# Kernel optimization log

Measured on AMD Instinct MI355X. Metric: run time of the kernel, lower is better.

The kernel has to match this reference:

```python
import jax, jax.numpy as jnp
import numpy as np
from jax import lax

BN_EPS = 1e-5
TINY = 1e-12


def conv2d(x, w, stride, padding):
    # NCHW x OIHW -> NCHW
    return lax.conv_general_dilated(
        x, w, (stride, stride), [(padding, padding), (padding, padding)],
        dimension_numbers=('NCHW', 'OIHW', 'NCHW'))


def pool2x2(x):
    B, C, H, W = x.shape
    return x.reshape(B, C, H // 2, 2, W // 2, 2).mean(axis=(3, 5))


def setup_inputs() -> dict:
    key = jax.random.key(0)
    k0, k1, k2, k3 = jax.random.split(key, 4)
    B, Cin, H, W = 32, 128, 56, 56
    Cout, K = 256, 3
    mean = jax.random.normal(k0, (B, Cin, H, W), jnp.float32)
    std = jax.random.uniform(k1, (B, Cin, H, W), jnp.float32)  # std must be >= 0
    fan_in = Cin * K * K
    bound = 1.0 / np.sqrt(fan_in)  # torch Conv2d default init
    conv_w = jax.random.uniform(k2, (Cout, Cin, K, K), jnp.float32, -bound, bound)
    conv_b = jax.random.uniform(k3, (Cout,), jnp.float32, -bound, bound)
    bn_gamma = jnp.full((Cout,), 2.5, jnp.float32)  # module fills weight with 2.5
    bn_beta = jnp.full((Cout,), 2.5, jnp.float32)   # module fills bias with 2.5
    return {'mean': mean, 'std': std, 'conv_w': conv_w, 'conv_b': conv_b,
            'bn_gamma': bn_gamma, 'bn_beta': bn_beta}


def reference(mean, std, conv_w, conv_b, bn_gamma, bn_beta):
    # mean branch: standard conv
    m = conv2d(mean, conv_w, 1, 1) + conv_b[None, :, None, None]
    # std branch (no rho): independent-variance propagation, var -> conv with w^2
    var = conv2d(std * std, conv_w * conv_w, 1, 1)
    s = jnp.sqrt(var + TINY)
    # BatchNorm2d in training mode: batch statistics over (N, H, W)
    mu = jnp.mean(m, axis=(0, 2, 3), keepdims=True)
    v = jnp.var(m, axis=(0, 2, 3), keepdims=True)  # biased, like torch normalization
    inv = 1.0 / jnp.sqrt(v + BN_EPS)
    g = bn_gamma[None, :, None, None]
    uhat = (m - mu) * inv * g + bn_beta[None, :, None, None]
    # std through BN: pure linear scale by |gamma| / sqrt(var + eps)
    shat = s * inv * jnp.abs(g)
    # moment activation (erf-based Gaussian->Heaviside moment mapping)
    z = uhat / (shat * np.sqrt(2.0) + TINY)
    u = 0.5 * (1.0 + lax.erf(z))               # output mean in (0, 1)
    sa = jnp.sqrt(jnp.clip(u * (1.0 - u), TINY))  # output std of Bernoulli-like moments
    # avg-pool 2x2 stride 2: mean pools linearly, independent vars: std = sqrt(avg(var))/2
    u_p = pool2x2(u)
    s_p = jnp.sqrt(pool2x2(sa * sa)) * 0.5
    return (u_p, s_p)
```

## Files before the change

### kernel.cpp

```cpp
#include <hip/hip_runtime.h>
#include <hip/hip_bf16.h>
#include <math.h>

#define BB 32
#define CIN 128
#define HH 56
#define WW 56
#define COUT 256
#define HW (HH*WW)
#define NPIX (BB*HW)
#define PH 28
#define PW 28
#define POOL_ELEMS ((long)BB*COUT*PH*PW)
#define PADH 58
#define PADW 58
#define TRANS_BLOCKS ((BB*PADH*PADW*16)/256)
#define WPACK_BLOCKS ((9*COUT*CIN)/256)

typedef unsigned short u16;
using s16x8 = __attribute__((ext_vector_type(8))) short;
using s16x4 = __attribute__((ext_vector_type(4))) short;
using f32x4 = __attribute__((ext_vector_type(4))) float;

__device__ __forceinline__ float b2f(u16 u){ return __uint_as_float(((unsigned)u)<<16); }
__device__ __forceinline__ u16 f2b(float x){
    unsigned u = __float_as_uint(x);
    unsigned r = (u + 0x7fffu + ((u>>16)&1u)) >> 16;
    return (u16)r;
}

__device__ __forceinline__ void gload16(const void* g, void* l){
    __builtin_amdgcn_global_load_lds(
        (const __attribute__((address_space(1))) unsigned int*)g,
        (__attribute__((address_space(3))) unsigned int*)l, 16, 0, 0);
}


__global__ __launch_bounds__(256) void prep_kernel(
    const float* __restrict__ mean, const float* __restrict__ stdv,
    const float* __restrict__ w,
    u16* __restrict__ mean_pad, u16* __restrict__ std2_pad,
    u16* __restrict__ BP, u16* __restrict__ BP2)
{
    int bid = blockIdx.x;
    if (bid < TRANS_BLOCKS){
        int t   = bid*256 + threadIdx.x;
        int oct = t & 15;
        int pp  = t >> 4;
        int pw = pp % PADW; int tmp = pp / PADW;
        int ph = tmp % PADH; int b = tmp / PADH;
        size_t obase = (size_t)pp*CIN + oct*8;
        s16x8 pm = (s16x8){0,0,0,0,0,0,0,0}, ps = pm;
        if (ph >= 1 && ph <= HH && pw >= 1 && pw <= WW){
            long ibase = ((long)(b*CIN + oct*8)*HH + (ph-1))*WW + (pw-1);
            #pragma unroll
            for (int j=0;j<8;j++){
                float m = mean[ibase + (long)j*HW];
                float s = stdv[ibase + (long)j*HW];
                pm[j] = (short)f2b(m);
                ps[j] = (short)f2b(s*s);
            }
        }
        *(s16x8*)(mean_pad + obase) = pm;
        *(s16x8*)(std2_pad + obase) = ps;
    } else {
        int t = (bid - TRANS_BLOCKS)*256 + threadIdx.x;
        int e    = t & 7;
        int co   = (t >> 3) & 255;
        int rest = t >> 11;
        int ks   = rest >> 2;
        int sub  = rest & 3;
        int r    = ks >> 2;
        int ci   = (ks & 3)*32 + sub*8 + e;
        float v = w[((long)co*CIN + ci)*9 + r];
        BP[t]  = f2b(v);
        BP2[t] = f2b(v*v);
    }
}

__global__ __launch_bounds__(256,2) void convw_kernel(
    const u16* __restrict__ mean_pad, const u16* __restrict__ std2_pad,
    const u16* __restrict__ BP, const u16* __restrict__ BP2,
    const float* __restrict__ bias,
    u16* __restrict__ m_out, u16* __restrict__ v_out,
    float* __restrict__ sum_, float* __restrict__ sumsq_)
{
    __shared__ u16 lds[32768];
    const int tid  = threadIdx.x;
    const int lane = tid & 63;
    const int wv   = tid >> 6;

    int gid   = blockIdx.x;
    int local = gid >> 3;
    int p     = (gid & 7)*112 + (local >> 1);
    int path  = local & 1;
    const int b  = p / 28;
    const int h0 = (p - b*28) * 2;

    const u16* __restrict__ Ap = path ? std2_pad : mean_pad;
    const u16* __restrict__ Bp = path ? BP2      : BP;
    u16*       __restrict__ Op = path ? v_out    : m_out;

    const int slot_g = (tid & 15) ^ ((tid >> 4) & 15);
    const int wbase  = (b*PADH + h0)*PADW*CIN;
    const int athr   = (tid >> 4)*CIN + slot_g*8;
    #pragma unroll
    for (int i=0; i<16; ++i){
        const int Ci = (i>>2)*(PADW*CIN) + (i&3)*16*CIN;
        gload16(Ap + wbase + Ci + athr, &lds[i*2048 + tid*8]);
    }
    __syncthreads();

    int R0[7];
    #pragma unroll
    for (int mi=0; mi<7; ++mi){
        int px = mi*16 + (lane & 15);
        int dh = (px >= 56) ? 1 : 0;
        R0[mi] = dh*64 + (px - dh*56);
    }
    const int q = lane >> 4;

    const u16* bp = Bp + (size_t)((lane>>4)*256 + wv*64 + (lane&15))*8;

    f32x4 acc[7][4];
    #pragma unroll
    for (int i=0;i<7;i++)
      #pragma unroll
      for (int j=0;j<4;j++) acc[i][j] = (f32x4){0,0,0,0};

    #pragma unroll
    for (int r=0; r<9; ++r){
        const int kh = r/3, kw = r - (r/3)*3;

        int ab[7];
        #pragma unroll
        for (int mi=0; mi<7; ++mi){
            int R   = R0[mi] + kh*64 + kw;
            int t15 = (R0[mi] + kw) & 15;
            ab[mi] = R*128 + ((q ^ t15) << 3);
        }

        #pragma unroll
        for (int hf=0; hf<2; ++hf){
            #pragma unroll
            for (int kk=0; kk<2; ++kk){
                const size_t ksoff = (size_t)(r*4 + hf*2 + kk)*8192;
                s16x8 bf0 = *(const s16x8*)(bp + ksoff);
                s16x8 bf1 = *(const s16x8*)(bp + ksoff + 128);
                s16x8 bf2 = *(const s16x8*)(bp + ksoff + 256);
                s16x8 bf3 = *(const s16x8*)(bp + ksoff + 384);
                const int sx = hf*64 + kk*32;
                s16x8 af[7];
                #pragma unroll
                for (int mi=0; mi<7; ++mi)
                    af[mi] = *(const s16x8*)&lds[ab[mi] ^ sx];
                __builtin_amdgcn_s_setprio(1);
                #pragma unroll
                for (int mi=0; mi<7; ++mi){
                    acc[mi][0] = __builtin_amdgcn_mfma_f32_16x16x32_bf16(af[mi], bf0, acc[mi][0], 0,0,0);
                    acc[mi][1] = __builtin_amdgcn_mfma_f32_16x16x32_bf16(af[mi], bf1, acc[mi][1], 0,0,0);
                    acc[mi][2] = __builtin_amdgcn_mfma_f32_16x16x32_bf16(af[mi], bf2, acc[mi][2], 0,0,0);
                    acc[mi][3] = __builtin_amdgcn_mfma_f32_16x16x32_bf16(af[mi], bf3, acc[mi][3], 0,0,0);
                }
                __builtin_amdgcn_s_setprio(0);
            }
        }
    }

    float bv[4];
    if (path == 0){
        #pragma unroll
        for (int ni=0;ni<4;ni++) bv[ni] = bias[wv*64 + ni*16 + (lane&15)];
    } else {
        #pragma unroll
        for (int ni=0;ni<4;ni++) bv[ni] = 0.f;
    }

    float ssum[4] = {0.f,0.f,0.f,0.f}, ssq[4] = {0.f,0.f,0.f,0.f};

    #pragma unroll
    for (int mi=0; mi<7; ++mi){
        int px = mi*16 + ((lane>>4)<<2);
        int dh = (px >= 56) ? 1 : 0;
        int w  = px - dh*56;
        #pragma unroll
        for (int ni=0; ni<4; ++ni){
            int co = wv*64 + ni*16 + (lane&15);
            size_t o = (size_t)(b*COUT + co)*HW + (size_t)(h0+dh)*WW + w;
            s16x4 pk;
            #pragma unroll
            for (int rr=0; rr<4; ++rr){
                float vv = acc[mi][ni][rr] + bv[ni];
                pk[rr] = (short)f2b(vv);
                ssum[ni] += vv;
                ssq[ni]  += vv*vv;
            }
            *(s16x4*)(Op + o) = pk;
        }
    }

    if (path == 0){
        #pragma unroll
        for (int ni=0; ni<4; ++ni){
            float s = ssum[ni], s2 = ssq[ni];
            s  += __shfl_xor(s, 16, 64);  s2 += __shfl_xor(s2, 16, 64);
            s  += __shfl_xor(s, 32, 64);  s2 += __shfl_xor(s2, 32, 64);
            if (lane < 16){
                int co = wv*64 + ni*16 + lane;
                atomicAdd(&sum_[co],   s);
                atomicAdd(&sumsq_[co], s2);
            }
        }
    }
}

__global__ __launch_bounds__(256) void final_kernel(
        const u16* __restrict__ m, const u16* __restrict__ var,
        const float* __restrict__ sum_, const float* __restrict__ sumsq_,
        const float* __restrict__ gamma, const float* __restrict__ beta,
        float* __restrict__ out){
    int idx4 = blockIdx.x*256 + threadIdx.x;
    int wo4 = idx4 % (PW/4); int t = idx4 / (PW/4);
    int ho = t % PH; t /= PH;
    int co = t % COUT; int b = t / COUT;
    float g  = gamma[co];
    float be = beta[co];
    float mu = sum_[co] / (float)NPIX;
    float vr = sumsq_[co] / (float)NPIX - mu*mu;
    float inv = 1.0f / sqrtf(vr + 1e-5f);
    float ag = fabsf(g);
    float us[4] = {0.f,0.f,0.f,0.f}, ss[4] = {0.f,0.f,0.f,0.f};
    #pragma unroll
    for (int dh=0; dh<2; ++dh){
        long base = ((long)(b*COUT+co)*HH + 2*ho+dh)*WW + wo4*8;
        const s16x8 vm = *(const s16x8*)&m[base];
        const s16x8 vv = *(const s16x8*)&var[base];
        #pragma unroll
        for (int j=0;j<8;j++){
            float mm = b2f((u16)vm[j]);
            float sdev = sqrtf(b2f((u16)vv[j]) + 1e-12f);
            float uhat = (mm - mu)*inv*g + be;
            float shat = sdev*inv*ag;
            float z = uhat / (shat*1.41421356237f + 1e-12f);
            float u = 0.5f*(1.f + erff(z));
            us[j>>1] += u;
            ss[j>>1] += fmaxf(u*(1.f-u), 1e-12f);
        }
    }
    long ob = ((long)(b*COUT+co)*PH + ho)*PW + wo4*4;
    f32x4 o0, o1;
    #pragma unroll
    for (int k=0;k<4;k++){
        o0[k] = 0.25f*us[k];
        o1[k] = sqrtf(0.25f*ss[k])*0.5f;
    }
    *(f32x4*)(out + ob) = o0;
    *(f32x4*)(out + POOL_ELEMS + ob) = o1;
}


__global__ void wtransf_kernel(const float* __restrict__ w, float* __restrict__ wT){
    int out = blockIdx.x*256 + threadIdx.x;
    if (out >= COUT*CIN*9) return;
    int co = out % COUT;
    int r  = out / COUT;
    wT[out] = w[(long)co*(CIN*9) + r];
}

__global__ __launch_bounds__(256) void stats_old_kernel(const u16* __restrict__ m,
        float* __restrict__ mu_out, float* __restrict__ inv_out){
    int co = blockIdx.x;
    float s=0.f, s2=0.f;
    for (int oc = threadIdx.x; oc < NPIX/8; oc += 256){
        int b = oc / (HW/8); int o8 = oc - b*(HW/8);
        const s16x8 v8 = *(const s16x8*)&m[((size_t)(b*COUT+co))*HW + (size_t)o8*8];
        #pragma unroll
        for (int j=0;j<8;j++){ float v = b2f((u16)v8[j]); s += v; s2 += v*v; }
    }
    __shared__ float rs[256], rs2[256];
    rs[threadIdx.x]=s; rs2[threadIdx.x]=s2; __syncthreads();
    for (int o=128;o>0;o>>=1){
        if (threadIdx.x < o){ rs[threadIdx.x]+=rs[threadIdx.x+o]; rs2[threadIdx.x]+=rs2[threadIdx.x+o]; }
        __syncthreads();
    }
    if (threadIdx.x==0){
        float mu = rs[0]/(float)NPIX;
        float var = rs2[0]/(float)NPIX - mu*mu;
        mu_out[co] = mu;
        inv_out[co] = 1.0f/sqrtf(var + 1e-5f);
    }
}

__global__ __launch_bounds__(256) void final_old_kernel(
        const u16* __restrict__ m, const u16* __restrict__ var,
        const float* __restrict__ mu_, const float* __restrict__ inv_,
        const float* __restrict__ gamma, const float* __restrict__ beta,
        float* __restrict__ out){
    long idx = (long)blockIdx.x*256 + threadIdx.x;
    int wo = (int)(idx % PW); long t = idx / PW;
    int ho = (int)(t % PH); t /= PH;
    int co = (int)(t % COUT); int b = (int)(t / COUT);
    float g  = gamma[co];
    float be = beta[co];
    float mu = mu_[co], inv = inv_[co];
    float ag = fabsf(g);
    float us = 0.f, ss = 0.f;
    #pragma unroll
    for (int dh=0; dh<2; ++dh){
        int hpos = 2*ho+dh;
        long base = ((long)(b*COUT+co)*HH + hpos)*WW + 2*wo;
        #pragma unroll
        for (int dw=0; dw<2; ++dw){
            float mm = b2f(m[base+dw]);
            float vv = b2f(var[base+dw]);
            float sdev = sqrtf(vv + 1e-12f);
            float uhat = (mm - mu)*inv*g + be;
            float shat = sdev*inv*ag;
            float z = uhat / (shat*1.41421356237f + 1e-12f);
            float u = 0.5f*(1.f + erff(z));
            float sa2 = fmaxf(u*(1.f-u), 1e-12f);
            us += u; ss += sa2;
        }
    }
    out[idx]              = 0.25f*us;
    out[POOL_ELEMS + idx] = sqrtf(0.25f*ss)*0.5f;
}

#define CI_CHUNK 64
#define XW 32
__global__ __launch_bounds__(256) void conv_old_kernel(
    const float* __restrict__ mean, const float* __restrict__ stdv,
    const float* __restrict__ wT, const float* __restrict__ bias,
    u16* __restrict__ m_out, u16* __restrict__ v_out)
{
    __shared__ float lds_m[CI_CHUNK][3][XW];
    __shared__ float lds_s[CI_CHUNK][3][XW];
    const int co   = threadIdx.x;
    const int half = blockIdx.x;
    const int h    = blockIdx.y;
    const int b    = blockIdx.z;
    const int w_base = half*28;

    float acc_m[28], acc_v[28];
    #pragma unroll
    for (int i=0;i<28;i++){ acc_m[i]=0.f; acc_v[i]=0.f; }

    for (int c=0; c<CIN; c+=CI_CHUNK){
        for (int t = threadIdx.x; t < CI_CHUNK*3*30; t += 256){
            int pos = t % 30; int r = t / 30; int hh = r % 3; int ci_l = r / 3;
            int gh = h - 1 + hh; int gw = w_base - 1 + pos;
            float vm = 0.f, vs = 0.f;
            if ((unsigned)gh < (unsigned)HH && (unsigned)gw < (unsigned)WW){
                long gi = ((long)(b*CIN + (c+ci_l))*HH + gh)*WW + gw;
                vm = mean[gi];
                float sv = stdv[gi];
                vs = sv*sv;
            }
            lds_m[ci_l][hh][pos] = vm;
            lds_s[ci_l][hh][pos] = vs;
        }
        __syncthreads();
        for (int ci_l=0; ci_l<CI_CHUNK; ++ci_l){
            int rbase = (c+ci_l)*9;
            #pragma unroll
            for (int kh=0; kh<3; ++kh){
                float w0 = wT[(long)(rbase + kh*3 + 0)*COUT + co];
                float w1 = wT[(long)(rbase + kh*3 + 1)*COUT + co];
                float w2 = wT[(long)(rbase + kh*3 + 2)*COUT + co];
                float xm[30];
                #pragma unroll
                for (int p=0;p<30;p++) xm[p] = lds_m[ci_l][kh][p];
                #pragma unroll
                for (int i=0;i<28;i++) acc_m[i] += w0*xm[i] + w1*xm[i+1] + w2*xm[i+2];
                float q0=w0*w0, q1=w1*w1, q2=w2*w2;
                float xs[30];
                #pragma unroll
                for (int p=0;p<30;p++) xs[p] = lds_s[ci_l][kh][p];
                #pragma unroll
                for (int i=0;i<28;i++) acc_v[i] += q0*xs[i] + q1*xs[i+1] + q2*xs[i+2];
            }
        }
        __syncthreads();
    }
    float bvv = bias[co];
    long obase = ((long)(b*COUT+co)*HH + h)*WW + w_base;
    #pragma unroll
    for (int i=0;i<28;i++){
        m_out[obase+i] = f2b(acc_m[i]+bvv);
        v_out[obase+i] = f2b(acc_v[i]);
    }
}

extern "C" void kernel_launch(void* const* d_in, const int* in_sizes, int n_in,
                              void* d_out, int out_size, void* d_ws, size_t ws_size,
                              hipStream_t stream)
{
    const float* mean   = (const float*)d_in[0];
    const float* stdv   = (const float*)d_in[1];
    const float* conv_w = (const float*)d_in[2];
    const float* conv_b = (const float*)d_in[3];
    const float* gamma  = (const float*)d_in[4];
    const float* beta   = (const float*)d_in[5];
    float* out = (float*)d_out;
    char* ws = (char*)d_ws;

    const size_t PAD_BYTES  = (size_t)BB*PADH*PADW*CIN*2;
    const size_t SLACK      = 8192;
    const size_t OFF_STD2   = PAD_BYTES + SLACK;
    const size_t OFF_WT     = OFF_STD2 + PAD_BYTES + SLACK;
    const size_t WT_BYTES   = (size_t)9*COUT*CIN*2;
    const size_t OFF_WT2    = OFF_WT + WT_BYTES;
    const size_t OFF_M      = OFF_WT2 + WT_BYTES;
    const size_t MV_BYTES   = (size_t)BB*COUT*HW*2;
    const size_t OFF_V      = OFF_M + MV_BYTES;
    const size_t OFF_SUM    = OFF_V + MV_BYTES;
    const size_t OFF_SUMSQ  = OFF_SUM + 1024;
    const size_t NEED_FAST  = OFF_SUMSQ + 1024;

    if (ws_size >= NEED_FAST){
        u16* mean_pad = (u16*)ws;
        u16* std2_pad = (u16*)(ws + OFF_STD2);
        u16* BP   = (u16*)(ws + OFF_WT);
        u16* BP2  = (u16*)(ws + OFF_WT2);
        u16* m_buf = (u16*)(ws + OFF_M);
        u16* v_buf = (u16*)(ws + OFF_V);
        float* sum_   = (float*)(ws + OFF_SUM);
        float* sumsq_ = (float*)(ws + OFF_SUMSQ);

        hipMemsetAsync(ws + OFF_SUM, 0, 2048, stream);
        prep_kernel<<<TRANS_BLOCKS + WPACK_BLOCKS, 256, 0, stream>>>(
            mean, stdv, conv_w, mean_pad, std2_pad, BP, BP2);
        convw_kernel<<<(NPIX/112)*2, 256, 0, stream>>>(
            mean_pad, std2_pad, BP, BP2, conv_b, m_buf, v_buf, sum_, sumsq_);
        final_kernel<<<(int)(POOL_ELEMS/4/256), 256, 0, stream>>>(
            m_buf, v_buf, sum_, sumsq_, gamma, beta, out);
    } else {
        u16* m_buf = (u16*)ws;
        u16* v_buf = (u16*)(ws + (size_t)BB*COUT*HW*2);
        float* wT  = (float*)(ws + (size_t)BB*COUT*HW*4);
        float* mu  = (float*)(ws + (size_t)BB*COUT*HW*4 + (size_t)COUT*CIN*9*4);
        float* inv = mu + 256;
        wtransf_kernel<<<(COUT*CIN*9+255)/256, 256, 0, stream>>>(conv_w, wT);
        conv_old_kernel<<<dim3(2, HH, BB), 256, 0, stream>>>(mean, stdv, wT, conv_b, m_buf, v_buf);
        stats_old_kernel<<<COUT, 256, 0, stream>>>(m_buf, mu, inv);
        final_old_kernel<<<(int)(POOL_ELEMS/256), 256, 0, stream>>>(m_buf, v_buf, mu, inv, gamma, beta, out);
    }
}
```

Baseline: 229.8 us.

## Transpose input via LDS per row with coalesced loads and fold memset into prep

The NCHW-to-padded-NHWC bf16 transpose now runs one block per (batch, row). Each block loads float4-coalesced input into swizzled LDS, then writes 16-byte NHWC vectors. Separate blocks zero the top and bottom pad rows, and the prep kernel also zeroes the BN sum buffers, which removes the hipMemsetAsync call. This is meant to replace strided scalar global reads with coalesced ones and drop one launch, at the cost of LDS use and a barrier in the prep kernel.

New measurement: 205.0 us, median of 3. 10.8% less time.

```diff
diff --git a/kernel.cpp b/kernel.cpp
--- a/kernel.cpp
+++ b/kernel.cpp
@@ -14,7 +14,8 @@
 #define POOL_ELEMS ((long)BB*COUT*PH*PW)
 #define PADH 58
 #define PADW 58
-#define TRANS_BLOCKS ((BB*PADH*PADW*16)/256)
+#define ROW_BLOCKS (BB*HH)
+#define TOPBOT_BLOCKS (BB*2)
 #define WPACK_BLOCKS ((9*COUT*CIN)/256)
 
 typedef unsigned short u16;
@@ -40,41 +41,88 @@
     const float* __restrict__ mean, const float* __restrict__ stdv,
     const float* __restrict__ w,
     u16* __restrict__ mean_pad, u16* __restrict__ std2_pad,
-    u16* __restrict__ BP, u16* __restrict__ BP2)
+    u16* __restrict__ BP, u16* __restrict__ BP2,
+    float* __restrict__ sum_, float* __restrict__ sumsq_)
 {
-    int bid = blockIdx.x;
-    if (bid < TRANS_BLOCKS){
-        int t   = bid*256 + threadIdx.x;
-        int oct = t & 15;
-        int pp  = t >> 4;
-        int pw = pp % PADW; int tmp = pp / PADW;
-        int ph = tmp % PADH; int b = tmp / PADH;
-        size_t obase = (size_t)pp*CIN + oct*8;
-        s16x8 pm = (s16x8){0,0,0,0,0,0,0,0}, ps = pm;
-        if (ph >= 1 && ph <= HH && pw >= 1 && pw <= WW){
-            long ibase = ((long)(b*CIN + oct*8)*HH + (ph-1))*WW + (pw-1);
+    const int bid = blockIdx.x;
+    const int t   = threadIdx.x;
+
+    if (bid < ROW_BLOCKS){
+        __shared__ u16 ldsm[56*128];
+        __shared__ u16 ldss[56*128];
+        const int b = bid / HH;
+        const int h = bid - b*HH;
+
+        #pragma unroll
+        for (int k=0; k<7; ++k){
+            int idx = k*256 + t;
+            int c   = idx / 14;
+            int f4  = idx - c*14;
+            long ga = ((long)(b*CIN + c)*HH + h)*WW + f4*4;
+            const f32x4 m4 = *(const f32x4*)(mean + ga);
+            const f32x4 s4 = *(const f32x4*)(stdv + ga);
             #pragma unroll
-            for (int j=0;j<8;j++){
-                float m = mean[ibase + (long)j*HW];
-                float s = stdv[ibase + (long)j*HW];
-                pm[j] = (short)f2b(m);
-                ps[j] = (short)f2b(s*s);
-            }
-        }
-        *(s16x8*)(mean_pad + obase) = pm;
-        *(s16x8*)(std2_pad + obase) = ps;
+            for (int j=0; j<4; ++j){
+                int px = f4*4 + j;
+                int ci = px*128 + (c ^ ((px & 15) << 3));
+                ldsm[ci] = f2b(m4[j]);
+                ldss[ci] = f2b(s4[j] * s4[j]);
+            }
+        }
+        __syncthreads();
+
+        const long rowbase = ((long)(b*PADH + (h+1)))*PADW*CIN;
+        #pragma unroll
+        for (int k=0; k<4; ++k){
+            int slot = k*256 + t;
+            int px   = slot >> 4;
+            int oct  = slot & 15;
+            if (px < 56){
+                int ci = px*128 + ((oct ^ (px & 15)) << 3);
+                long o = rowbase + (long)(px+1)*CIN + oct*8;
+                *(s16x8*)(mean_pad + o) = *(const s16x8*)&ldsm[ci];
+                *(s16x8*)(std2_pad + o) = *(const s16x8*)&ldss[ci];
+            }
+        }
+        if (t < 64){
+            int buf = t >> 5;
+            int ppx = ((t >> 4) & 1) ? 57 : 0;
+            int oct = t & 15;
+            long o  = rowbase + (long)ppx*CIN + oct*8;
+            s16x8 z = (s16x8){0,0,0,0,0,0,0,0};
+            *(s16x8*)((buf ? std2_pad : mean_pad) + o) = z;
+        }
+    } else if (bid < ROW_BLOCKS + TOPBOT_BLOCKS){
+        int row = bid - ROW_BLOCKS;
+        int b   = row >> 1;
+        int ph  = (row & 1) ? (PADH-1) : 0;
+        const long rowbase = ((long)(b*PADH + ph))*PADW*CIN;
+        s16x8 z = (s16x8){0,0,0,0,0,0,0,0};
+        #pragma unroll
+        for (int k=0; k<8; ++k){
+            int g = k*256 + t;
+            if (g < 2*PADW*16){
+                int buf = g >= PADW*16;
+                int gg  = buf ? g - PADW*16 : g;
+                int px  = gg >> 4;
+                int oct = gg & 15;
+                long o  = rowbase + (long)px*CIN + oct*8;
+                *(s16x8*)((buf ? std2_pad : mean_pad) + o) = z;
+            }
+        }
+        if (row == 0){ sum_[t] = 0.f; sumsq_[t] = 0.f; }
     } else {
-        int t = (bid - TRANS_BLOCKS)*256 + threadIdx.x;
-        int e    = t & 7;
-        int co   = (t >> 3) & 255;
-        int rest = t >> 11;
+        int tt = (bid - ROW_BLOCKS - TOPBOT_BLOCKS)*256 + t;
+        int e    = tt & 7;
+        int co   = (tt >> 3) & 255;
+        int rest = tt >> 11;
         int ks   = rest >> 2;
         int sub  = rest & 3;
         int r    = ks >> 2;
         int ci   = (ks & 3)*32 + sub*8 + e;
         float v = w[((long)co*CIN + ci)*9 + r];
-        BP[t]  = f2b(v);
-        BP2[t] = f2b(v*v);
+        BP[tt]  = f2b(v);
+        BP2[tt] = f2b(v*v);
     }
 }
 
@@ -427,9 +475,8 @@
         float* sum_   = (float*)(ws + OFF_SUM);
         float* sumsq_ = (float*)(ws + OFF_SUMSQ);
 
-        hipMemsetAsync(ws + OFF_SUM, 0, 2048, stream);
-        prep_kernel<<<TRANS_BLOCKS + WPACK_BLOCKS, 256, 0, stream>>>(
-            mean, stdv, conv_w, mean_pad, std2_pad, BP, BP2);
+        prep_kernel<<<ROW_BLOCKS + TOPBOT_BLOCKS + WPACK_BLOCKS, 256, 0, stream>>>(
+            mean, stdv, conv_w, mean_pad, std2_pad, BP, BP2, sum_, sumsq_);
         convw_kernel<<<(NPIX/112)*2, 256, 0, stream>>>(
             mean_pad, std2_pad, BP, BP2, conv_b, m_buf, v_buf, sum_, sumsq_);
         final_kernel<<<(int)(POOL_ELEMS/4/256), 256, 0, stream>>>(
```
